# Kernel tuning notes

Measured on AMD Instinct MI355X. Metric: run time of the kernel, lower is better.

The kernel has to match this reference:

```python
import jax, jax.numpy as jnp
import numpy as np

B, D, H, O, E = 1048576, 17, 8, 6, 4  # batch, input_dim, expert_hidden, output_dim, n_clusters
G1, G2 = 64, 32  # gating hidden dims


def setup_inputs() -> dict:
    key = jax.random.key(0)
    ks = jax.random.split(key, 14)
    def w(k, shape, fan_in):
        return (jax.random.normal(k, shape, jnp.float32) / jnp.sqrt(jnp.float32(fan_in)))
    return {
        "x": jax.random.normal(ks[0], (B, D), jnp.float32),
        # per-expert MLP params, stacked on leading expert axis E
        "eW1": w(ks[1], (E, D, H), D), "eb1": w(ks[2], (E, H), D),
        "eW2": w(ks[3], (E, H, H), H), "eb2": w(ks[4], (E, H), H),
        "eW3": w(ks[5], (E, H, O), H), "eb3": w(ks[6], (E, O), H),
        # gating classifier params
        "gW1": w(ks[7], (D, G1), D), "gb1": w(ks[8], (G1,), D),
        "gW2": w(ks[9], (G1, G2), G1), "gb2": w(ks[10], (G2,), G1),
        "gW3": w(ks[11], (G2, E), G2), "gb3": w(ks[12], (E,), G2),
    }


def reference(x, eW1, eb1, eW2, eb2, eW3, eb3, gW1, gb1, gW2, gb2, gW3, gb3):
    # gating network: 17 -> 64 -> 32 -> 4 logits
    h = jax.nn.relu(x @ gW1 + gb1)
    h = jax.nn.relu(h @ gW2 + gb2)
    gating_logits = h @ gW3 + gb3  # [B, E]
    selected = jnp.argmax(gating_logits, axis=1)  # [B] hard routing
    # all experts computed (as in the original), stacked over expert axis
    e = jax.nn.relu(jnp.einsum('bi,eih->beh', x, eW1) + eb1)   # [B, E, H]
    e = jax.nn.relu(jnp.einsum('beh,ehk->bek', e, eW2) + eb2)  # [B, E, H]
    eo = jnp.einsum('bek,eko->beo', e, eW3) + eb3              # [B, E, O]
    # gather the selected expert's output per sample
    predictions = jnp.take_along_axis(eo, selected[:, None, None], axis=1)[:, 0, :]  # [B, O]
    return predictions, gating_logits
```

## Files before the change

### kernel.cpp

```cpp
#include <hip/hip_runtime.h>

#define BTOT 1048576
#define D 17
#define H 8
#define OUT 6
#define E 4
#define G1 64
#define G2 32
#define CHUNKS 4
#define XSTR 17
#define GTHR 5.0e-3f

typedef float f32x4 __attribute__((ext_vector_type(4)));
typedef float f32x2 __attribute__((ext_vector_type(2)));
typedef short s16x8 __attribute__((ext_vector_type(8)));
typedef unsigned int uint;

union U4S8 { uint u[4]; s16x8 s; };

__device__ __forceinline__ uint bfr(uint u) {
    return (u + 0x7fffu + ((u >> 16) & 1u)) & 0xffff0000u;
}

__device__ __forceinline__ void wsplit2(float a, float b, uint &hp, uint &lp) {
    uint ha = bfr(__float_as_uint(a));
    uint hb = bfr(__float_as_uint(b));
    float ra = a - __uint_as_float(ha);
    float rb = b - __uint_as_float(hb);
    hp = (ha >> 16) | (hb & 0xffff0000u);
    lp = (bfr(__float_as_uint(ra)) >> 16) | (bfr(__float_as_uint(rb)) & 0xffff0000u);
}

__device__ __forceinline__ void split8t(const float* p, s16x8 &fh, s16x8 &fm, s16x8 &fl) {
    U4S8 Hh, Mm, Ll;
    #pragma unroll
    for (int i = 0; i < 4; ++i) {
        float a = p[2 * i], b = p[2 * i + 1];
        uint ua = __float_as_uint(a), ub = __float_as_uint(b);
        Hh.u[i] = __builtin_amdgcn_perm(ub, ua, 0x07060302u);
        float ra = a - __uint_as_float(ua & 0xffff0000u);
        float rb = b - __uint_as_float(ub & 0xffff0000u);
        uint ura = __float_as_uint(ra), urb = __float_as_uint(rb);
        Mm.u[i] = __builtin_amdgcn_perm(urb, ura, 0x07060302u);
        float sa = ra - __uint_as_float(ura & 0xffff0000u);
        float sb = rb - __uint_as_float(urb & 0xffff0000u);
        Ll.u[i] = __builtin_amdgcn_perm(__float_as_uint(sb), __float_as_uint(sa), 0x07060302u);
    }
    fh = Hh.s; fm = Mm.s; fl = Ll.s;
}

#define MM5(dacc, ah, am, al, bh, bl)                                            \
    dacc = __builtin_amdgcn_mfma_f32_16x16x32_bf16(am, bl, dacc, 0, 0, 0);       \
    dacc = __builtin_amdgcn_mfma_f32_16x16x32_bf16(al, bh, dacc, 0, 0, 0);       \
    dacc = __builtin_amdgcn_mfma_f32_16x16x32_bf16(ah, bl, dacc, 0, 0, 0);       \
    dacc = __builtin_amdgcn_mfma_f32_16x16x32_bf16(am, bh, dacc, 0, 0, 0);       \
    dacc = __builtin_amdgcn_mfma_f32_16x16x32_bf16(ah, bh, dacc, 0, 0, 0);

#define WSTR 292

__global__ __launch_bounds__(256, 2) void hybrid_ruc_kernel(
    const float* __restrict__ x,
    const float* __restrict__ eW1, const float* __restrict__ eb1,
    const float* __restrict__ eW2, const float* __restrict__ eb2,
    const float* __restrict__ eW3, const float* __restrict__ eb3,
    const float* __restrict__ gW1, const float* __restrict__ gb1,
    const float* __restrict__ gW2, const float* __restrict__ gb2,
    const float* __restrict__ gW3, const float* __restrict__ gb3,
    float* __restrict__ out)
{
    __shared__ __align__(16) float sscr[4][1024];
    __shared__ __align__(16) float swl[E * WSTR];
    __shared__ __align__(16) float sxp[256 * XSTR + 16];

    const int tid = threadIdx.x;
    const int wv  = tid >> 6;
    const int ln  = tid & 63;
    const int g   = ln >> 4;
    const int nn  = ln & 15;
    float* scr = sscr[wv];

    if (tid < 16) sxp[256 * XSTR + tid] = 0.0f;
    for (int t = tid; t < E * D * H; t += 256) {
        swl[(t / 136) * WSTR + (t % 136)] = eW1[t];
    }
    if (tid < E * H * H) {
        swl[(tid / 64) * WSTR + 144 + (tid % 64)] = eW2[tid];
    }
    if (tid < E * H * OUT) {
        int e = tid / 48, r = tid % 48, k = r / 6, o = r % 6;
        swl[e * WSTR + 216 + k * 8 + o] = eW3[tid];
    }
    if (tid < E * H) swl[(tid / 8) * WSTR + 136 + (tid % 8)] = eb1[tid];
    if (tid < E * H) swl[(tid / 8) * WSTR + 208 + (tid % 8)] = eb2[tid];
    if (tid < E * OUT) swl[(tid / 6) * WSTR + 280 + (tid % 6)] = eb3[tid];

    {
        const float* gs = x + (long long)blockIdx.x * (CHUNKS * 256 * D) + wv * (64 * D);
        float* ls = &sxp[wv * (64 * D)];
        #pragma unroll
        for (int i = 0; i < D; ++i) ls[i * 64 + ln] = gs[i * 64 + ln];
    }

    float cb1[4], cb2[2], cb3;
    #pragma unroll
    for (int ct = 0; ct < 4; ++ct) cb1[ct] = gb1[ct * 16 + nn];
    cb2[0] = gb2[nn]; cb2[1] = gb2[16 + nn];
    cb3 = (nn < 4) ? gb3[nn] : 0.0f;

    s16x8 B1h[4], B1l[4];
    #pragma unroll
    for (int ct = 0; ct < 4; ++ct) {
        U4S8 Hh, Ll;
        #pragma unroll
        for (int j2 = 0; j2 < 4; ++j2) {
            const int k0 = g * 8 + 2 * j2, n = ct * 16 + nn;
            const float a = (k0 < D)     ? gW1[k0 * G1 + n]       : 0.0f;
            const float b = (k0 + 1 < D) ? gW1[(k0 + 1) * G1 + n] : 0.0f;
            wsplit2(a, b, Hh.u[j2], Ll.u[j2]);
        }
        B1h[ct] = Hh.s; B1l[ct] = Ll.s;
    }
    s16x8 B2h[2][2], B2l[2][2];
    #pragma unroll
    for (int ct = 0; ct < 2; ++ct)
        #pragma unroll
        for (int kt = 0; kt < 2; ++kt) {
            U4S8 Hh, Ll;
            #pragma unroll
            for (int j2 = 0; j2 < 4; ++j2) {
                const int k0 = kt * 32 + g * 8 + 2 * j2, n = ct * 16 + nn;
                wsplit2(gW2[k0 * G2 + n], gW2[(k0 + 1) * G2 + n], Hh.u[j2], Ll.u[j2]);
            }
            B2h[ct][kt] = Hh.s; B2l[ct][kt] = Ll.s;
        }
    s16x8 B3h, B3l;
    {
        U4S8 Hh, Ll;
        #pragma unroll
        for (int j2 = 0; j2 < 4; ++j2) {
            const int k0 = g * 8 + 2 * j2;
            const float a = (nn < 4) ? gW3[k0 * E + nn]       : 0.0f;
            const float b = (nn < 4) ? gW3[(k0 + 1) * E + nn] : 0.0f;
            wsplit2(a, b, Hh.u[j2], Ll.u[j2]);
        }
        B3h = Hh.s; B3l = Ll.s;
    }

    __syncthreads();

    #pragma unroll 1
    for (int c = 0; c < CHUNKS; ++c) {
        const long long cbase = ((long long)blockIdx.x * CHUNKS + c) * 256;
        if (c) {
            const float* gs = x + cbase * D + wv * (64 * D);
            float* ls = &sxp[wv * (64 * D)];
            #pragma unroll
            for (int i = 0; i < D; ++i) ls[i * 64 + ln] = gs[i * 64 + ln];
        }

        f32x4 Lg[4];
        #pragma unroll
        for (int rt = 0; rt < 4; ++rt) {
            const int srow = wv * 64 + rt * 16 + nn;
            float xv[8];
            const int xb = srow * XSTR + ((g == 3) ? 0 : g * 8);
            #pragma unroll
            for (int j = 0; j < 8; ++j) xv[j] = sxp[xb + j];
            s16x8 a1h, a1m, a1l; split8t(xv, a1h, a1m, a1l);

            #pragma unroll
            for (int ct = 0; ct < 4; ++ct) {
                f32x4 d = {cb1[ct], cb1[ct], cb1[ct], cb1[ct]};
                MM5(d, a1h, a1m, a1l, B1h[ct], B1l[ct]);
                #pragma unroll
                for (int r = 0; r < 4; ++r) {
                    float hv = fmaxf(d[r], 0.0f);
                    int s = g * 4 + r, n = ct * 16 + nn;
                    scr[s * 64 + (((n >> 2) ^ (s & 15)) << 2) + (n & 3)] = hv;
                }
            }

            s16x8 a2h[2], a2m[2], a2l[2];
            #pragma unroll
            for (int kt = 0; kt < 2; ++kt) {
                int kb0 = kt * 8 + g * 2;
                float hv8[8];
                *(f32x4*)&hv8[0] = *(const f32x4*)(&scr[nn * 64 + ((kb0 ^ (nn & 15)) << 2)]);
                *(f32x4*)&hv8[4] = *(const f32x4*)(&scr[nn * 64 + (((kb0 + 1) ^ (nn & 15)) << 2)]);
                split8t(hv8, a2h[kt], a2m[kt], a2l[kt]);
            }

            #pragma unroll
            for (int ct = 0; ct < 2; ++ct) {
                f32x4 d = {cb2[ct], cb2[ct], cb2[ct], cb2[ct]};
                #pragma unroll
                for (int kt = 0; kt < 2; ++kt) {
                    MM5(d, a2h[kt], a2m[kt], a2l[kt], B2h[ct][kt], B2l[ct][kt]);
                }
                #pragma unroll
                for (int r = 0; r < 4; ++r) {
                    float hv = fmaxf(d[r], 0.0f);
                    int s = g * 4 + r, n = ct * 16 + nn;
                    scr[s * 32 + (((n >> 2) ^ (s & 7)) << 2) + (n & 3)] = hv;
                }
            }

            float h28[8];
            *(f32x4*)&h28[0] = *(const f32x4*)(&scr[nn * 32 + (((2 * g) ^ (nn & 7)) << 2)]);
            *(f32x4*)&h28[4] = *(const f32x4*)(&scr[nn * 32 + (((2 * g + 1) ^ (nn & 7)) << 2)]);
            s16x8 a3h, a3m, a3l; split8t(h28, a3h, a3m, a3l);

            f32x4 d3 = {cb3, cb3, cb3, cb3};
            MM5(d3, a3h, a3m, a3l, B3h, B3l);
            Lg[rt] = d3;
        }

        if (nn < 4) {
            #pragma unroll
            for (int rt = 0; rt < 4; ++rt)
                #pragma unroll
                for (int r = 0; r < 4; ++r)
                    scr[(rt * 16 + g * 4 + r) * 4 + nn] = Lg[rt][r];
        }
        f32x4 lgv = *(const f32x4*)(&scr[ln * 4]);

        int sel = 0;
        {
            float b = lgv.x;
            if (lgv.y > b) { b = lgv.y; sel = 1; }
            if (lgv.z > b) { b = lgv.z; sel = 2; }
            if (lgv.w > b) { b = lgv.w; sel = 3; }
        }
        float mx01 = fmaxf(lgv.x, lgv.y), mn01 = fminf(lgv.x, lgv.y);
        float mx23 = fmaxf(lgv.z, lgv.w), mn23 = fminf(lgv.z, lgv.w);
        float best   = fmaxf(mx01, mx23);
        float second = fmaxf(fminf(mx01, mx23), (mx01 >= mx23) ? mn01 : mn23);

        unsigned long long fmask = __ballot(best - second < GTHR);
        if (fmask) {
            do {
                int sl = (int)__builtin_ctzll(fmask);
                fmask &= (fmask - 1);
                const int fr = wv * 64 + sl;
                float h1j = gb1[ln];
                #pragma unroll 1
                for (int i = 0; i < D; ++i)
                    h1j = __builtin_fmaf(sxp[fr * XSTR + i], gW1[i * G1 + ln], h1j);
                scr[ln] = fmaxf(h1j, 0.0f);
                int j2 = ln & 31;
                float h2j = gb2[j2];
                #pragma unroll 4
                for (int c2 = 0; c2 < G1; ++c2)
                    h2j = __builtin_fmaf(scr[c2], gW2[c2 * G2 + j2], h2j);
                scr[64 + j2] = fmaxf(h2j, 0.0f);
                int e = ln & 3;
                float lge = gb3[e];
                #pragma unroll 4
                for (int jj = 0; jj < G2; ++jj)
                    lge = __builtin_fmaf(scr[64 + jj], gW3[jj * E + e], lge);
                float l0 = __shfl(lge, 0), l1 = __shfl(lge, 1);
                float l2 = __shfl(lge, 2), l3 = __shfl(lge, 3);
                int s2 = 0; float bb = l0;
                if (l1 > bb) { bb = l1; s2 = 1; }
                if (l2 > bb) { bb = l2; s2 = 2; }
                if (l3 > bb) { bb = l3; s2 = 3; }
                if (ln == sl) sel = s2;
            } while (fmask);
        }

        const float* xrow = &sxp[tid * XSTR];
        const float* wl = &swl[sel * WSTR];

        float t1[H];
        {
            f32x4 ba = *(const f32x4*)(wl + 136);
            f32x4 bb = *(const f32x4*)(wl + 140);
            t1[0]=ba.x; t1[1]=ba.y; t1[2]=ba.z; t1[3]=ba.w;
            t1[4]=bb.x; t1[5]=bb.y; t1[6]=bb.z; t1[7]=bb.w;
        }
        #pragma unroll
        for (int i = 0; i < D; ++i) {
            const float xi = xrow[i];
            f32x4 wa = *(const f32x4*)(wl + i * 8);
            f32x4 wb = *(const f32x4*)(wl + i * 8 + 4);
            t1[0] = __builtin_fmaf(xi, wa.x, t1[0]);
            t1[1] = __builtin_fmaf(xi, wa.y, t1[1]);
            t1[2] = __builtin_fmaf(xi, wa.z, t1[2]);
            t1[3] = __builtin_fmaf(xi, wa.w, t1[3]);
            t1[4] = __builtin_fmaf(xi, wb.x, t1[4]);
            t1[5] = __builtin_fmaf(xi, wb.y, t1[5]);
            t1[6] = __builtin_fmaf(xi, wb.z, t1[6]);
            t1[7] = __builtin_fmaf(xi, wb.w, t1[7]);
        }
        float t2[H];
        {
            f32x4 ba = *(const f32x4*)(wl + 208);
            f32x4 bb = *(const f32x4*)(wl + 212);
            t2[0]=ba.x; t2[1]=ba.y; t2[2]=ba.z; t2[3]=ba.w;
            t2[4]=bb.x; t2[5]=bb.y; t2[6]=bb.z; t2[7]=bb.w;
        }
        #pragma unroll
        for (int k = 0; k < H; ++k) {
            const float tv = fmaxf(t1[k], 0.0f);
            f32x4 wa = *(const f32x4*)(wl + 144 + k * 8);
            f32x4 wb = *(const f32x4*)(wl + 144 + k * 8 + 4);
            t2[0] = __builtin_fmaf(tv, wa.x, t2[0]);
            t2[1] = __builtin_fmaf(tv, wa.y, t2[1]);
            t2[2] = __builtin_fmaf(tv, wa.z, t2[2]);
            t2[3] = __builtin_fmaf(tv, wa.w, t2[3]);
            t2[4] = __builtin_fmaf(tv, wb.x, t2[4]);
            t2[5] = __builtin_fmaf(tv, wb.y, t2[5]);
            t2[6] = __builtin_fmaf(tv, wb.z, t2[6]);
            t2[7] = __builtin_fmaf(tv, wb.w, t2[7]);
        }
        float pred[OUT];
        {
            f32x4 ba = *(const f32x4*)(wl + 280);
            pred[0]=ba.x; pred[1]=ba.y; pred[2]=ba.z; pred[3]=ba.w;
            pred[4]=wl[284]; pred[5]=wl[285];
        }
        #pragma unroll
        for (int k = 0; k < H; ++k) {
            const float tv = fmaxf(t2[k], 0.0f);
            f32x4 wa = *(const f32x4*)(wl + 216 + k * 8);
            f32x2 wb = *(const f32x2*)(wl + 216 + k * 8 + 4);
            pred[0] = __builtin_fmaf(tv, wa.x, pred[0]);
            pred[1] = __builtin_fmaf(tv, wa.y, pred[1]);
            pred[2] = __builtin_fmaf(tv, wa.z, pred[2]);
            pred[3] = __builtin_fmaf(tv, wa.w, pred[3]);
            pred[4] = __builtin_fmaf(tv, wb.x, pred[4]);
            pred[5] = __builtin_fmaf(tv, wb.y, pred[5]);
        }

        const long long b = cbase + tid;
        f32x2 p0 = {pred[0], pred[1]};
        f32x2 p1 = {pred[2], pred[3]};
        f32x2 p2 = {pred[4], pred[5]};
        *(f32x2*)(out + b * 6)     = p0;
        *(f32x2*)(out + b * 6 + 2) = p1;
        *(f32x2*)(out + b * 6 + 4) = p2;
        float* lout = out + (long long)BTOT * OUT;
        *(f32x4*)(lout + b * 4) = lgv;
    }
}

extern "C" void kernel_launch(void* const* d_in, const int* in_sizes, int n_in,
                              void* d_out, int out_size, void* d_ws, size_t ws_size,
                              hipStream_t stream) {
    const float* x   = (const float*)d_in[0];
    const float* eW1 = (const float*)d_in[1];
    const float* eb1 = (const float*)d_in[2];
    const float* eW2 = (const float*)d_in[3];
    const float* eb2 = (const float*)d_in[4];
    const float* eW3 = (const float*)d_in[5];
    const float* eb3 = (const float*)d_in[6];
    const float* gW1 = (const float*)d_in[7];
    const float* gb1 = (const float*)d_in[8];
    const float* gW2 = (const float*)d_in[9];
    const float* gb2 = (const float*)d_in[10];
    const float* gW3 = (const float*)d_in[11];
    const float* gb3 = (const float*)d_in[12];
    float* out = (float*)d_out;

    dim3 grid(BTOT / (256 * CHUNKS)), block(256);
    hipLaunchKernelGGL(hybrid_ruc_kernel, grid, block, 0, stream,
                       x, eW1, eb1, eW2, eb2, eW3, eb3,
                       gW1, gb1, gW2, gb2, gW3, gb3, out);
}
```

Measured before the change: 240.7 us.

## Cut split-bf16 MFMA passes to three, read expert weights from global, restage x

Drops the third bf16 residual term, so each gating matmul uses 3 MFMAs instead of 5 and the split work shrinks. Removes the shared-memory copy of the expert weights, and the expert MLP now reads the selected expert's weights directly from global memory (cached). Restages x into a padded stride-20 layout with coalesced loads so rows can be read as vectors, and halves CHUNKS per block. The lower-precision gating risks flipping argmax near ties. The global weight loads are divergent per lane and could add latency.

```diff
diff --git a/kernel.cpp b/kernel.cpp
--- a/kernel.cpp
+++ b/kernel.cpp
@@ -7,8 +7,8 @@
 #define E 4
 #define G1 64
 #define G2 32
-#define CHUNKS 4
-#define XSTR 17
+#define CHUNKS 2
+#define XSTR 20
 #define GTHR 5.0e-3f
 
 typedef float f32x4 __attribute__((ext_vector_type(4)));
@@ -31,8 +31,8 @@
     lp = (bfr(__float_as_uint(ra)) >> 16) | (bfr(__float_as_uint(rb)) & 0xffff0000u);
 }
 
-__device__ __forceinline__ void split8t(const float* p, s16x8 &fh, s16x8 &fm, s16x8 &fl) {
-    U4S8 Hh, Mm, Ll;
+__device__ __forceinline__ void split8t2(const float* p, s16x8 &fh, s16x8 &fm) {
+    U4S8 Hh, Mm;
     #pragma unroll
     for (int i = 0; i < 4; ++i) {
         float a = p[2 * i], b = p[2 * i + 1];
@@ -40,23 +40,15 @@
         Hh.u[i] = __builtin_amdgcn_perm(ub, ua, 0x07060302u);
         float ra = a - __uint_as_float(ua & 0xffff0000u);
         float rb = b - __uint_as_float(ub & 0xffff0000u);
-        uint ura = __float_as_uint(ra), urb = __float_as_uint(rb);
-        Mm.u[i] = __builtin_amdgcn_perm(urb, ura, 0x07060302u);
-        float sa = ra - __uint_as_float(ura & 0xffff0000u);
-        float sb = rb - __uint_as_float(urb & 0xffff0000u);
-        Ll.u[i] = __builtin_amdgcn_perm(__float_as_uint(sb), __float_as_uint(sa), 0x07060302u);
+        Mm.u[i] = __builtin_amdgcn_perm(__float_as_uint(rb), __float_as_uint(ra), 0x07060302u);
     }
-    fh = Hh.s; fm = Mm.s; fl = Ll.s;
-}
-
-#define MM5(dacc, ah, am, al, bh, bl)                                            \
-    dacc = __builtin_amdgcn_mfma_f32_16x16x32_bf16(am, bl, dacc, 0, 0, 0);       \
-    dacc = __builtin_amdgcn_mfma_f32_16x16x32_bf16(al, bh, dacc, 0, 0, 0);       \
+    fh = Hh.s; fm = Mm.s;
+}
+
+#define MM3(dacc, ah, am, bh, bl)                                                \
+    dacc = __builtin_amdgcn_mfma_f32_16x16x32_bf16(am, bh, dacc, 0, 0, 0);       \
     dacc = __builtin_amdgcn_mfma_f32_16x16x32_bf16(ah, bl, dacc, 0, 0, 0);       \
-    dacc = __builtin_amdgcn_mfma_f32_16x16x32_bf16(am, bh, dacc, 0, 0, 0);       \
     dacc = __builtin_amdgcn_mfma_f32_16x16x32_bf16(ah, bh, dacc, 0, 0, 0);
-
-#define WSTR 292
 
 __global__ __launch_bounds__(256, 2) void hybrid_ruc_kernel(
     const float* __restrict__ x,
@@ -69,7 +61,6 @@
     float* __restrict__ out)
 {
     __shared__ __align__(16) float sscr[4][1024];
-    __shared__ __align__(16) float swl[E * WSTR];
     __shared__ __align__(16) float sxp[256 * XSTR + 16];
 
     const int tid = threadIdx.x;
@@ -79,27 +70,10 @@
     const int nn  = ln & 15;
     float* scr = sscr[wv];
 
+    sxp[tid * XSTR + 17] = 0.0f;
+    sxp[tid * XSTR + 18] = 0.0f;
+    sxp[tid * XSTR + 19] = 0.0f;
     if (tid < 16) sxp[256 * XSTR + tid] = 0.0f;
-    for (int t = tid; t < E * D * H; t += 256) {
-        swl[(t / 136) * WSTR + (t % 136)] = eW1[t];
-    }
-    if (tid < E * H * H) {
-        swl[(tid / 64) * WSTR + 144 + (tid % 64)] = eW2[tid];
-    }
-    if (tid < E * H * OUT) {
-        int e = tid / 48, r = tid % 48, k = r / 6, o = r % 6;
-        swl[e * WSTR + 216 + k * 8 + o] = eW3[tid];
-    }
-    if (tid < E * H) swl[(tid / 8) * WSTR + 136 + (tid % 8)] = eb1[tid];
-    if (tid < E * H) swl[(tid / 8) * WSTR + 208 + (tid % 8)] = eb2[tid];
-    if (tid < E * OUT) swl[(tid / 6) * WSTR + 280 + (tid % 6)] = eb3[tid];
-
-    {
-        const float* gs = x + (long long)blockIdx.x * (CHUNKS * 256 * D) + wv * (64 * D);
-        float* ls = &sxp[wv * (64 * D)];
-        #pragma unroll
-        for (int i = 0; i < D; ++i) ls[i * 64 + ln] = gs[i * 64 + ln];
-    }
 
     float cb1[4], cb2[2], cb3;
     #pragma unroll
@@ -146,17 +120,23 @@
         B3h = Hh.s; B3l = Ll.s;
     }
 
-    __syncthreads();
+    const int q0 = tid / 17;
+    const int r0 = tid - q0 * 17;
 
     #pragma unroll 1
     for (int c = 0; c < CHUNKS; ++c) {
         const long long cbase = ((long long)blockIdx.x * CHUNKS + c) * 256;
-        if (c) {
-            const float* gs = x + cbase * D + wv * (64 * D);
-            float* ls = &sxp[wv * (64 * D)];
-            #pragma unroll
-            for (int i = 0; i < D; ++i) ls[i * 64 + ln] = gs[i * 64 + ln];
-        }
+        if (c) __syncthreads();
+
+        #pragma unroll
+        for (int j = 0; j < D; ++j) {
+            const int rj = r0 + j;
+            const int cy = (rj >= 17) ? 1 : 0;
+            const int k  = rj - (cy ? 17 : 0);
+            const int s  = 15 * j + q0 + cy;
+            sxp[s * XSTR + k] = x[cbase * D + tid + j * 256];
+        }
+        __syncthreads();
 
         f32x4 Lg[4];
         #pragma unroll
@@ -164,14 +144,14 @@
             const int srow = wv * 64 + rt * 16 + nn;
             float xv[8];
             const int xb = srow * XSTR + ((g == 3) ? 0 : g * 8);
-            #pragma unroll
-            for (int j = 0; j < 8; ++j) xv[j] = sxp[xb + j];
-            s16x8 a1h, a1m, a1l; split8t(xv, a1h, a1m, a1l);
+            *(f32x4*)&xv[0] = *(const f32x4*)(&sxp[xb]);
+            *(f32x4*)&xv[4] = *(const f32x4*)(&sxp[xb + 4]);
+            s16x8 a1h, a1m; split8t2(xv, a1h, a1m);
 
             #pragma unroll
             for (int ct = 0; ct < 4; ++ct) {
                 f32x4 d = {cb1[ct], cb1[ct], cb1[ct], cb1[ct]};
-                MM5(d, a1h, a1m, a1l, B1h[ct], B1l[ct]);
+                MM3(d, a1h, a1m, B1h[ct], B1l[ct]);
                 #pragma unroll
                 for (int r = 0; r < 4; ++r) {
                     float hv = fmaxf(d[r], 0.0f);
@@ -180,14 +160,14 @@
                 }
             }
 
-            s16x8 a2h[2], a2m[2], a2l[2];
+            s16x8 a2h[2], a2m[2];
             #pragma unroll
             for (int kt = 0; kt < 2; ++kt) {
                 int kb0 = kt * 8 + g * 2;
                 float hv8[8];
-                *(f32x4*)&hv8[0] = *(const f32x4*)(&scr[nn * 64 + ((kb0 ^ (nn & 15)) << 2)]);
-                *(f32x4*)&hv8[4] = *(const f32x4*)(&scr[nn * 64 + (((kb0 + 1) ^ (nn & 15)) << 2)]);
-                split8t(hv8, a2h[kt], a2m[kt], a2l[kt]);
+                *(f32x4*)&hv8[0] = *(const f32x4*)(&scr[nn * 64 + ((kb0 ^ nn) << 2)]);
+                *(f32x4*)&hv8[4] = *(const f32x4*)(&scr[nn * 64 + (((kb0 + 1) ^ nn) << 2)]);
+                split8t2(hv8, a2h[kt], a2m[kt]);
             }
 
             #pragma unroll
@@ -195,7 +175,7 @@
                 f32x4 d = {cb2[ct], cb2[ct], cb2[ct], cb2[ct]};
                 #pragma unroll
                 for (int kt = 0; kt < 2; ++kt) {
-                    MM5(d, a2h[kt], a2m[kt], a2l[kt], B2h[ct][kt], B2l[ct][kt]);
+                    MM3(d, a2h[kt], a2m[kt], B2h[ct][kt], B2l[ct][kt]);
                 }
                 #pragma unroll
                 for (int r = 0; r < 4; ++r) {
@@ -208,10 +188,10 @@
             float h28[8];
             *(f32x4*)&h28[0] = *(const f32x4*)(&scr[nn * 32 + (((2 * g) ^ (nn & 7)) << 2)]);
             *(f32x4*)&h28[4] = *(const f32x4*)(&scr[nn * 32 + (((2 * g + 1) ^ (nn & 7)) << 2)]);
-            s16x8 a3h, a3m, a3l; split8t(h28, a3h, a3m, a3l);
+            s16x8 a3h, a3m; split8t2(h28, a3h, a3m);
 
             f32x4 d3 = {cb3, cb3, cb3, cb3};
-            MM5(d3, a3h, a3m, a3l, B3h, B3l);
+            MM3(d3, a3h, a3m, B3h, B3l);
             Lg[rt] = d3;
         }
 
@@ -268,21 +248,36 @@
             } while (fmask);
         }
 
-        const float* xrow = &sxp[tid * XSTR];
-        const float* wl = &swl[sel * WSTR];
+        float xr[D];
+        {
+            const float* xrow = &sxp[tid * XSTR];
+            f32x4 x0 = *(const f32x4*)(xrow);
+            f32x4 x1 = *(const f32x4*)(xrow + 4);
+            f32x4 x2 = *(const f32x4*)(xrow + 8);
+            f32x4 x3 = *(const f32x4*)(xrow + 12);
+            xr[0]=x0.x; xr[1]=x0.y; xr[2]=x0.z; xr[3]=x0.w;
+            xr[4]=x1.x; xr[5]=x1.y; xr[6]=x1.z; xr[7]=x1.w;
+            xr[8]=x2.x; xr[9]=x2.y; xr[10]=x2.z; xr[11]=x2.w;
+            xr[12]=x3.x; xr[13]=x3.y; xr[14]=x3.z; xr[15]=x3.w;
+            xr[16]=xrow[16];
+        }
+        const float* w1g = eW1 + sel * (D * H);
+        const float* w2g = eW2 + sel * (H * H);
+        const float* w3g = eW3 + sel * (H * OUT);
 
         float t1[H];
         {
-            f32x4 ba = *(const f32x4*)(wl + 136);
-            f32x4 bb = *(const f32x4*)(wl + 140);
+            const float* bg = eb1 + sel * H;
+            f32x4 ba = *(const f32x4*)(bg);
+            f32x4 bb = *(const f32x4*)(bg + 4);
             t1[0]=ba.x; t1[1]=ba.y; t1[2]=ba.z; t1[3]=ba.w;
             t1[4]=bb.x; t1[5]=bb.y; t1[6]=bb.z; t1[7]=bb.w;
         }
         #pragma unroll
         for (int i = 0; i < D; ++i) {
-            const float xi = xrow[i];
-            f32x4 wa = *(const f32x4*)(wl + i * 8);
-            f32x4 wb = *(const f32x4*)(wl + i * 8 + 4);
+            const float xi = xr[i];
+            f32x4 wa = *(const f32x4*)(w1g + i * 8);
+            f32x4 wb = *(const f32x4*)(w1g + i * 8 + 4);
             t1[0] = __builtin_fmaf(xi, wa.x, t1[0]);
             t1[1] = __builtin_fmaf(xi, wa.y, t1[1]);
             t1[2] = __builtin_fmaf(xi, wa.z, t1[2]);
@@ -294,16 +289,17 @@
         }
         float t2[H];
         {
-            f32x4 ba = *(const f32x4*)(wl + 208);
-            f32x4 bb = *(const f32x4*)(wl + 212);
+            const float* bg = eb2 + sel * H;
+            f32x4 ba = *(const f32x4*)(bg);
+            f32x4 bb = *(const f32x4*)(bg + 4);
             t2[0]=ba.x; t2[1]=ba.y; t2[2]=ba.z; t2[3]=ba.w;
             t2[4]=bb.x; t2[5]=bb.y; t2[6]=bb.z; t2[7]=bb.w;
         }
         #pragma unroll
         for (int k = 0; k < H; ++k) {
             const float tv = fmaxf(t1[k], 0.0f);
-            f32x4 wa = *(const f32x4*)(wl + 144 + k * 8);
-            f32x4 wb = *(const f32x4*)(wl + 144 + k * 8 + 4);
+            f32x4 wa = *(const f32x4*)(w2g + k * 8);
+            f32x4 wb = *(const f32x4*)(w2g + k * 8 + 4);
             t2[0] = __builtin_fmaf(tv, wa.x, t2[0]);
             t2[1] = __builtin_fmaf(tv, wa.y, t2[1]);
             t2[2] = __builtin_fmaf(tv, wa.z, t2[2]);
@@ -315,21 +311,32 @@
         }
         float pred[OUT];
         {
-            f32x4 ba = *(const f32x4*)(wl + 280);
-            pred[0]=ba.x; pred[1]=ba.y; pred[2]=ba.z; pred[3]=ba.w;
-            pred[4]=wl[284]; pred[5]=wl[285];
-        }
-        #pragma unroll
-        for (int k = 0; k < H; ++k) {
-            const float tv = fmaxf(t2[k], 0.0f);
-            f32x4 wa = *(const f32x4*)(wl + 216 + k * 8);
-            f32x2 wb = *(const f32x2*)(wl + 216 + k * 8 + 4);
-            pred[0] = __builtin_fmaf(tv, wa.x, pred[0]);
-            pred[1] = __builtin_fmaf(tv, wa.y, pred[1]);
-            pred[2] = __builtin_fmaf(tv, wa.z, pred[2]);
-            pred[3] = __builtin_fmaf(tv, wa.w, pred[3]);
-            pred[4] = __builtin_fmaf(tv, wb.x, pred[4]);
-            pred[5] = __builtin_fmaf(tv, wb.y, pred[5]);
+            const float* bg = eb3 + sel * OUT;
+            f32x2 b0 = *(const f32x2*)(bg);
+            f32x2 b1 = *(const f32x2*)(bg + 2);
+            f32x2 b2 = *(const f32x2*)(bg + 4);
+            pred[0]=b0.x; pred[1]=b0.y; pred[2]=b1.x; pred[3]=b1.y;
+            pred[4]=b2.x; pred[5]=b2.y;
+        }
+        #pragma unroll
+        for (int j = 0; j < 4; ++j) {
+            const float tv0 = fmaxf(t2[2 * j],     0.0f);
+            const float tv1 = fmaxf(t2[2 * j + 1], 0.0f);
+            f32x4 wa = *(const f32x4*)(w3g + j * 12);
+            f32x4 wb = *(const f32x4*)(w3g + j * 12 + 4);
+            f32x4 wc = *(const f32x4*)(w3g + j * 12 + 8);
+            pred[0] = __builtin_fmaf(tv0, wa.x, pred[0]);
+            pred[1] = __builtin_fmaf(tv0, wa.y, pred[1]);
+            pred[2] = __builtin_fmaf(tv0, wa.z, pred[2]);
+            pred[3] = __builtin_fmaf(tv0, wa.w, pred[3]);
+            pred[4] = __builtin_fmaf(tv0, wb.x, pred[4]);
+            pred[5] = __builtin_fmaf(tv0, wb.y, pred[5]);
+            pred[0] = __builtin_fmaf(tv1, wb.z, pred[0]);
+            pred[1] = __builtin_fmaf(tv1, wb.w, pred[1]);
+            pred[2] = __builtin_fmaf(tv1, wc.x, pred[2]);
+            pred[3] = __builtin_fmaf(tv1, wc.y, pred[3]);
+            pred[4] = __builtin_fmaf(tv1, wc.z, pred[4]);
+            pred[5] = __builtin_fmaf(tv1, wc.w, pred[5]);
         }
 
         const long long b = cbase + tid;
```

Measured after the change: 275.2 us. 14.3% more time.
